# Kernel tuning notes

Measured on AMD Instinct MI355X. Metric: run time of the kernel, lower is better.

## Reference

```python
import jax, jax.numpy as jnp
import numpy as np

H = 16        # num_attention_heads
D = 1024      # hidden_size
HD = D // H   # attention_head_size = 64

def setup_inputs() -> dict:
    key = jax.random.key(0)
    ks = jax.random.split(key, 5)
    scale = 0.02
    return {
        "hidden_states": jax.random.normal(ks[0], (4, 2048, D), dtype=jnp.float32),
        "attention_mask": jnp.zeros((4, 2048), dtype=jnp.float32),
        "Wq": jax.random.normal(ks[1], (D, D), dtype=jnp.float32) * scale,
        "bq": jnp.zeros((D,), dtype=jnp.float32),
        "Wk": jax.random.normal(ks[2], (D, D), dtype=jnp.float32) * scale,
        "bk": jnp.zeros((D,), dtype=jnp.float32),
        "Wv": jax.random.normal(ks[3], (D, D), dtype=jnp.float32) * scale,
        "bv": jnp.zeros((D,), dtype=jnp.float32),
    }

def _heads(x, B, S):
    # [B,S,D] -> [B,H,S,HD]
    return x.reshape(B, S, H, HD).transpose(0, 2, 1, 3)

def reference(hidden_states, attention_mask, Wq, bq, Wk, bk, Wv, bv):
    B, S, _ = hidden_states.shape
    q = _heads(hidden_states @ Wq + bq, B, S)
    k = _heads(hidden_states @ Wk + bk, B, S)
    v = _heads(hidden_states @ Wv + bv, B, S)
    # scores: [B,H,S,S]
    scores = jnp.einsum('bhqd,bhkd->bhqk', q, k) / jnp.sqrt(jnp.float32(HD))
    scores = scores + attention_mask[:, None, None, :]  # additive mask
    probs = jax.nn.softmax(scores, axis=-1)
    # dropout is identity in eval mode
    ctx = jnp.einsum('bhqk,bhkd->bhqd', probs, v)
    return ctx.transpose(0, 2, 1, 3).reshape(B, S, H * HD)
```

## Files before the change

kernel.cpp:

```cpp
#include <hip/hip_runtime.h>


typedef __bf16 bf16_t;
typedef __bf16 bf16x2 __attribute__((ext_vector_type(2)));
typedef __bf16 bf16x4 __attribute__((ext_vector_type(4)));
typedef __bf16 bf16x8 __attribute__((ext_vector_type(8)));
typedef float floatx16 __attribute__((ext_vector_type(16)));
typedef float floatx4 __attribute__((ext_vector_type(4)));
typedef float floatx2 __attribute__((ext_vector_type(2)));

__device__ __forceinline__ void glds16(const void* g, void* l) {
  __builtin_amdgcn_global_load_lds(
      (const __attribute__((address_space(1))) void*)g,
      (__attribute__((address_space(3))) void*)l, 16, 0, 0);
}

__device__ __forceinline__ float exp2_fast(float x) {
  return __builtin_amdgcn_exp2f(x);
}

__device__ __forceinline__ unsigned pk2(float a, float b) {
  union { bf16x2 v; unsigned u; } cv;
  cv.v[0] = (bf16_t)a; cv.v[1] = (bf16_t)b;
  return cv.u;
}

__device__ __forceinline__ void plane32(unsigned& a, unsigned& b) {
  asm("v_permlane32_swap_b32 %0, %1" : "+v"(a), "+v"(b));
}

__global__ __launch_bounds__(256) void k_prep(const float* __restrict__ X,
                                              bf16_t* __restrict__ Xb,
                                              const float* __restrict__ Wq,
                                              const float* __restrict__ Wk,
                                              const float* __restrict__ Wv,
                                              bf16_t* __restrict__ Wt) {
  int bid = blockIdx.x;
  if (bid < 8192) {
    int i = (bid * 256 + threadIdx.x) * 4;
    float4 v = *(const float4*)(X + i);
    bf16x4 o;
    o[0] = (bf16_t)v.x; o[1] = (bf16_t)v.y; o[2] = (bf16_t)v.z; o[3] = (bf16_t)v.w;
    *(bf16x4*)(Xb + i) = o;
  } else {
    int t = bid - 8192;
    int z = t >> 10, r2 = t & 1023;
    int bx = r2 & 31, by = r2 >> 5;
    const float* W = (z == 0) ? Wq : ((z == 1) ? Wk : Wv);
    bf16_t* dst = Wt + (size_t)z * 1048576;
    __shared__ float tt[32][33];
    int tx = threadIdx.x & 31, ty = threadIdx.x >> 5;
#pragma unroll
    for (int r = 0; r < 4; r++) {
      int k = by * 32 + ty + r * 8;
      tt[ty + r * 8][tx] = W[k * 1024 + bx * 32 + tx];
    }
    __syncthreads();
#pragma unroll
    for (int r = 0; r < 4; r++) {
      int n = bx * 32 + ty + r * 8;
      dst[(size_t)n * 1024 + by * 32 + tx] = (bf16_t)tt[tx][ty + r * 8];
    }
  }
}

#define QKV_STAGE_A(kt, slot)                                 \
  do {                                                        \
    bf16_t* sA_ = lds + (slot) * 24576;                       \
    bf16_t* sB_ = sA_ + 8192;                                 \
    glds16(gA0 + (kt) * 64, sA_ + dA0);                       \
    glds16(gA1 + (kt) * 64, sA_ + dA1);                       \
    glds16(gB0 + (kt) * 64, sB_ + dB0);                       \
  } while (0)
#define QKV_STAGE_B(kt, slot)                                 \
  do {                                                        \
    bf16_t* sA_ = lds + (slot) * 24576;                       \
    bf16_t* sB_ = sA_ + 8192;                                 \
    glds16(gB1 + (kt) * 64, sB_ + dB1);                       \
    glds16(gB2 + (kt) * 64, sB_ + dB2);                       \
    glds16(gB3 + (kt) * 64, sB_ + dB3);                       \
  } while (0)

__global__ __launch_bounds__(512, 2) void k_qkv(
    const bf16_t* __restrict__ Xb, const bf16_t* __restrict__ Wt,
    const float* __restrict__ bq, const float* __restrict__ bk,
    const float* __restrict__ bv, bf16_t* __restrict__ Qb,
    bf16_t* __restrict__ Kb, bf16_t* __restrict__ Vt) {
  extern __shared__ bf16_t lds[];
  int tid = threadIdx.x, wv = tid >> 6, lane = tid & 63;
  int wvv = wv & 3, half = wv >> 2;
  int quad = lane >> 4, l16 = lane & 15;
  int wm = wvv >> 1, wn = wvv & 1;

  int id = blockIdx.x;
  int x = id & 7, w = id >> 3;
  int bn = w >> 3, pm = w & 7;
  int bm = x * 8 + pm;
  size_t m0 = (size_t)bm * 128, n0 = (size_t)bn * 256;
  int wsel = bn >> 2;

  const bf16_t* Ab = Xb + m0 * 1024;
  const bf16_t* Bb = Wt + n0 * 1024;

  const bf16_t *gA0, *gA1, *gB0, *gB1, *gB2, *gB3;
  int dA0, dA1, dB0, dB1, dB2, dB3;
  {
    int r8 = lane >> 3, l8 = lane & 7;
    int jA0 = wv * 2, jA1 = wv * 2 + 1;
    int rA0 = jA0 * 8 + r8, rA1 = jA1 * 8 + r8;
    gA0 = Ab + (size_t)rA0 * 1024 + ((l8 ^ (rA0 & 7)) * 8);
    gA1 = Ab + (size_t)rA1 * 1024 + ((l8 ^ (rA1 & 7)) * 8);
    dA0 = jA0 * 512; dA1 = jA1 * 512;
    int jB = wv * 4;
    int rB0 = (jB + 0) * 8 + r8, rB1 = (jB + 1) * 8 + r8;
    int rB2 = (jB + 2) * 8 + r8, rB3 = (jB + 3) * 8 + r8;
    gB0 = Bb + (size_t)rB0 * 1024 + ((l8 ^ (rB0 & 7)) * 8);
    gB1 = Bb + (size_t)rB1 * 1024 + ((l8 ^ (rB1 & 7)) * 8);
    gB2 = Bb + (size_t)rB2 * 1024 + ((l8 ^ (rB2 & 7)) * 8);
    gB3 = Bb + (size_t)rB3 * 1024 + ((l8 ^ (rB3 & 7)) * 8);
    dB0 = (jB + 0) * 512; dB1 = (jB + 1) * 512;
    dB2 = (jB + 2) * 512; dB3 = (jB + 3) * 512;
  }

  int ofsA[2][4], ofsB[2][4];
#pragma unroll
  for (int s = 0; s < 2; s++)
#pragma unroll
    for (int rt = 0; rt < 4; rt++) {
      int rowa = wm * 64 + rt * 16 + l16;
      ofsA[s][rt] = rowa * 64 + (((4 * s + quad) ^ (rowa & 7)) * 8);
      int rowb = wn * 64 + rt * 16 + l16;
      ofsB[s][rt] = rowb * 64 + (((4 * s + quad) ^ (rowb & 7)) * 8);
    }

  floatx4 acc[4][4];
#pragma unroll
  for (int a = 0; a < 4; a++)
#pragma unroll
    for (int b = 0; b < 4; b++)
#pragma unroll
      for (int r = 0; r < 4; r++) acc[a][b][r] = 0.f;

  QKV_STAGE_A(0, 0); QKV_STAGE_B(0, 0);
  QKV_STAGE_A(1, 1); QKV_STAGE_B(1, 1);

#pragma unroll
  for (int t = 0; t < 16; ++t) {
    asm volatile("" ::: "memory");
    __builtin_amdgcn_s_barrier();
    if (t < 15) asm volatile("s_waitcnt vmcnt(6)" ::: "memory");
    else        asm volatile("s_waitcnt vmcnt(0)" ::: "memory");
    __builtin_amdgcn_sched_barrier(0);
    __builtin_amdgcn_s_barrier();
    asm volatile("" ::: "memory");

    const bf16_t* sA = lds + (t % 3) * 24576;
    const bf16_t* sBh = sA + 8192 + half * 8192;
    const bf16_t* fA = (wsel == 2) ? sBh : sA;
    const bf16_t* fB = (wsel == 2) ? sA : sBh;

    if (t + 2 < 16) QKV_STAGE_A(t + 2, (t + 2) % 3);
    {
      bf16x8 av[4], bw[4];
#pragma unroll
      for (int rt = 0; rt < 4; rt++) {
        av[rt] = *(const bf16x8*)(fA + ofsA[0][rt]);
        bw[rt] = *(const bf16x8*)(fB + ofsB[0][rt]);
      }
      __builtin_amdgcn_s_setprio(1);
#pragma unroll
      for (int rt = 0; rt < 4; rt++)
#pragma unroll
        for (int ct = 0; ct < 4; ct++)
          acc[rt][ct] = __builtin_amdgcn_mfma_f32_16x16x32_bf16(av[rt], bw[ct],
                                                               acc[rt][ct], 0, 0, 0);
      __builtin_amdgcn_s_setprio(0);
    }
    asm volatile("" ::: "memory");
    __builtin_amdgcn_s_barrier();
    asm volatile("" ::: "memory");

    if (t + 2 < 16) QKV_STAGE_B(t + 2, (t + 2) % 3);
    {
      bf16x8 av[4], bw[4];
#pragma unroll
      for (int rt = 0; rt < 4; rt++) {
        av[rt] = *(const bf16x8*)(fA + ofsA[1][rt]);
        bw[rt] = *(const bf16x8*)(fB + ofsB[1][rt]);
      }
      __builtin_amdgcn_s_setprio(1);
#pragma unroll
      for (int rt = 0; rt < 4; rt++)
#pragma unroll
        for (int ct = 0; ct < 4; ct++)
          acc[rt][ct] = __builtin_amdgcn_mfma_f32_16x16x32_bf16(av[rt], bw[ct],
                                                               acc[rt][ct], 0, 0, 0);
      __builtin_amdgcn_s_setprio(0);
    }
  }

  __syncthreads();
  bf16_t* shC = lds + half * 16384;
  int s0 = (int)(m0 & 2047), bb = (int)(m0 >> 11);
  int n0h = (int)(n0 & 1023) + half * 128;
  int hbase = n0h >> 6;
  int th = tid & 255;

  if (wsel == 2) {
#pragma unroll
    for (int rt = 0; rt < 4; rt++) {
#pragma unroll
      for (int r = 0; r < 4; r++) {
        int nl = wm * 64 + rt * 16 + quad * 4 + r;
        float bi = bv[n0h + nl];
#pragma unroll
        for (int ct = 0; ct < 4; ct++) {
          int ml = wn * 64 + ct * 16 + l16;
          shC[nl * 128 + ml] = (bf16_t)(acc[rt][ct][r] + bi);
        }
      }
    }
    __syncthreads();
#pragma unroll
    for (int p = 0; p < 8; p++) {
      int c = p * 256 + th;
      int nl = c >> 4, mo = (c & 15) * 8;
      bf16x8 vv = *(const bf16x8*)(shC + nl * 128 + mo);
      int hh = hbase + (nl >> 6), dd = nl & 63;
      *(bf16x8*)(Vt + (size_t)(bb * 16 + hh) * 131072 + (size_t)dd * 2048 + s0 + mo) = vv;
    }
  } else {
    const float* bias = (wsel == 0) ? bq : bk;
#pragma unroll
    for (int ct = 0; ct < 4; ct++) {
      int nl = wn * 64 + ct * 16 + l16;
      float bi = bias[n0h + nl];
#pragma unroll
      for (int rt = 0; rt < 4; rt++) {
#pragma unroll
        for (int r = 0; r < 4; r++) {
          int ml = wm * 64 + rt * 16 + quad * 4 + r;
          float v = acc[rt][ct][r] + bi;
          shC[ml * 128 + nl] =
              (wsel == 0) ? (bf16_t)(v * 0.18033688011117f) : (bf16_t)v;
        }
      }
    }
    __syncthreads();
    bf16_t* outp = (wsel == 0) ? Qb : Kb;
#pragma unroll
    for (int p = 0; p < 8; p++) {
      int c = p * 256 + th;
      int h = c >> 10, c1 = c & 1023;
      int ml = c1 >> 3, ko = (c1 & 7) * 8;
      bf16x8 vv = *(const bf16x8*)(shC + ml * 128 + h * 64 + ko);
      *(bf16x8*)(outp + (size_t)(bb * 16 + hbase + h) * 131072 +
                 (size_t)(s0 + ml) * 64 + ko) = vv;
    }
  }
}

__global__ __launch_bounds__(256, 2) void k_attn(const bf16_t* __restrict__ Qb,
                                                 const bf16_t* __restrict__ Kb,
                                                 const bf16_t* __restrict__ VtG,
                                                 const float* __restrict__ mask,
                                                 float* __restrict__ out) {
  __shared__ float smem[10240];
  bf16_t* lds = (bf16_t*)smem;
  float* mlds = smem + 8192;

  int tid = threadIdx.x, wq = tid >> 6, lane = tid & 63;
  int q5 = lane & 31, h5 = lane >> 5;

  int id = blockIdx.x;
  int x = id & 7, w = id >> 3;
  int bh = x * 8 + (w >> 3), qt = w & 7;
  int b = bh >> 4, hh = bh & 15;

  const bf16_t* Qp = Qb + (size_t)bh * 131072;
  const bf16_t* Kp = Kb + (size_t)bh * 131072;
  const bf16_t* Vp = VtG + (size_t)bh * 131072;
  const float* mp = mask + b * 2048;

#pragma unroll
  for (int j = 0; j < 2; j++) {
    float4 mv = *(const float4*)(mp + tid * 8 + j * 4);
    float4 sv;
    sv.x = mv.x * 1.4426950408890f - 12.0f;
    sv.y = mv.y * 1.4426950408890f - 12.0f;
    sv.z = mv.z * 1.4426950408890f - 12.0f;
    sv.w = mv.w * 1.4426950408890f - 12.0f;
    *(float4*)(mlds + tid * 8 + j * 4) = sv;
  }

  int q0 = qt * 256 + wq * 64;
  bf16x8 qf0[4], qf1[4];
#pragma unroll
  for (int s = 0; s < 4; s++) {
    qf0[s] = *(const bf16x8*)(Qp + (size_t)(q0 + q5) * 64 + s * 16 + h5 * 8);
    qf1[s] = *(const bf16x8*)(Qp + (size_t)(q0 + 32 + q5) * 64 + s * 16 + h5 * 8);
  }

  union { uint4 u; bf16x8 v; } qfe;
  qfe.u.x = h5 ? 0u : 0x00003f80u;
  qfe.u.y = 0u; qfe.u.z = 0u; qfe.u.w = 0u;

  int off[2][4];
#pragma unroll
  for (int j = 0; j < 2; j++)
#pragma unroll
    for (int s = 0; s < 4; s++)
      off[j][s] = (j * 32 + q5) * 64 + (((2 * s + h5) ^ (q5 & 7)) * 8);

  int r0 = wq * 16 + (lane >> 3);
  int slot = (lane & 7) ^ ((lane >> 3) & 7);
  const bf16_t* kg0 = Kp + (size_t)r0 * 64 + slot * 8;
  const bf16_t* kg1 = kg0 + 512;
  const bf16_t* vg0 = Vp + (size_t)r0 * 2048 + slot * 8;
  const bf16_t* vg1 = vg0 + 16384;
  int c0 = wq * 2;

  floatx16 zed;
#pragma unroll
  for (int r = 0; r < 16; r++) zed[r] = 0.f;

  floatx16 ov[4];
#pragma unroll
  for (int t2 = 0; t2 < 4; t2++)
#pragma unroll
    for (int r = 0; r < 16; r++) ov[t2][r] = 0.f;
  floatx2 pA0, pA1, pB0, pB1;
  pA0[0] = pA0[1] = pA1[0] = pA1[1] = 0.f;
  pB0[0] = pB0[1] = pB1[0] = pB1[1] = 0.f;

  {
    bf16_t* bK = lds;
    bf16_t* bV = lds + 4096;
    glds16(kg0, bK + c0 * 512); glds16(kg1, bK + c0 * 512 + 512);
    glds16(vg0, bV + c0 * 512); glds16(vg1, bV + c0 * 512 + 512);
    kg0 += 4096; kg1 += 4096; vg0 += 64; vg1 += 64;
  }

  for (int it = 0; it < 32; ++it) {
    int kk0 = it * 64, cur = it & 1;
    __syncthreads();
    if (it + 1 < 32) {
      bf16_t* bK = lds + (cur ^ 1) * 8192;
      bf16_t* bV = bK + 4096;
      glds16(kg0, bK + c0 * 512); glds16(kg1, bK + c0 * 512 + 512);
      glds16(vg0, bV + c0 * 512); glds16(vg1, bV + c0 * 512 + 512);
      kg0 += 4096; kg1 += 4096; vg0 += 64; vg1 += 64;
    }
    const bf16_t* bK = lds + cur * 8192;
    const bf16_t* bV = bK + 4096;

    union { uint4 u; bf16x8 v; } kfe[2];
    kfe[0].u.x = h5 ? 0u : pk2(mlds[kk0 + q5], 0.f);
    kfe[1].u.x = h5 ? 0u : pk2(mlds[kk0 + 32 + q5], 0.f);
    kfe[0].u.y = 0u; kfe[0].u.z = 0u; kfe[0].u.w = 0u;
    kfe[1].u.y = 0u; kfe[1].u.z = 0u; kfe[1].u.w = 0u;

#pragma unroll
    for (int tt = 0; tt < 2; tt++) {
      bf16x8 kf[4], vfa[2], vfb[2];
#pragma unroll
      for (int s = 0; s < 4; s++) kf[s] = *(const bf16x8*)(bK + off[tt][s]);
#pragma unroll
      for (int t2 = 0; t2 < 2; t2++) {
        vfa[t2] = *(const bf16x8*)(bV + off[t2][tt * 2]);
        vfb[t2] = *(const bf16x8*)(bV + off[t2][tt * 2 + 1]);
      }

      floatx16 a0, a1;
      __builtin_amdgcn_s_setprio(1);
      floatx16 mt = __builtin_amdgcn_mfma_f32_32x32x16_bf16(kfe[tt].v, qfe.v, zed, 0, 0, 0);
      a0 = __builtin_amdgcn_mfma_f32_32x32x16_bf16(kf[0], qf0[0], mt, 0, 0, 0);
      a1 = __builtin_amdgcn_mfma_f32_32x32x16_bf16(kf[0], qf1[0], mt, 0, 0, 0);
#pragma unroll
      for (int s = 1; s < 4; s++) {
        a0 = __builtin_amdgcn_mfma_f32_32x32x16_bf16(kf[s], qf0[s], a0, 0, 0, 0);
        a1 = __builtin_amdgcn_mfma_f32_32x32x16_bf16(kf[s], qf1[s], a1, 0, 0, 0);
      }
      __builtin_amdgcn_s_setprio(0);

#pragma unroll
      for (int sl = 0; sl < 2; sl++) {
        int base = sl * 8;
        float e0 = exp2_fast(a0[base + 0]);
        float e1 = exp2_fast(a0[base + 1]);
        float e2 = exp2_fast(a0[base + 2]);
        float e3 = exp2_fast(a0[base + 3]);
        float e4 = exp2_fast(a0[base + 4]);
        float e5 = exp2_fast(a0[base + 5]);
        float e6 = exp2_fast(a0[base + 6]);
        float e7 = exp2_fast(a0[base + 7]);
        floatx2 u0, u1;
        u0[0] = e0 + e4; u0[1] = e1 + e5; pA0 += u0;
        u1[0] = e2 + e6; u1[1] = e3 + e7; pA1 += u1;
        unsigned A0 = pk2(e0, e1), B0 = pk2(e2, e3);
        unsigned C0 = pk2(e4, e5), D0 = pk2(e6, e7);
        float f0 = exp2_fast(a1[base + 0]);
        float f1 = exp2_fast(a1[base + 1]);
        float f2 = exp2_fast(a1[base + 2]);
        float f3 = exp2_fast(a1[base + 3]);
        float f4 = exp2_fast(a1[base + 4]);
        float f5 = exp2_fast(a1[base + 5]);
        float f6 = exp2_fast(a1[base + 6]);
        float f7 = exp2_fast(a1[base + 7]);
        floatx2 w0, w1;
        w0[0] = f0 + f4; w0[1] = f1 + f5; pB0 += w0;
        w1[0] = f2 + f6; w1[1] = f3 + f7; pB1 += w1;
        unsigned A1 = pk2(f0, f1), B1 = pk2(f2, f3);
        unsigned C1 = pk2(f4, f5), D1 = pk2(f6, f7);
        unsigned px0 = A0, pz0 = C0; plane32(px0, pz0);
        unsigned py0 = B0, pw0 = D0; plane32(py0, pw0);
        unsigned px1 = A1, pz1 = C1; plane32(px1, pz1);
        unsigned py1 = B1, pw1 = D1; plane32(py1, pw1);
        union { uint4 u; bf16x8 v; } pf0, pf1;
        pf0.u.x = px0; pf0.u.y = py0; pf0.u.z = pz0; pf0.u.w = pw0;
        pf1.u.x = px1; pf1.u.y = py1; pf1.u.z = pz1; pf1.u.w = pw1;
        __builtin_amdgcn_s_setprio(1);
#pragma unroll
        for (int t2 = 0; t2 < 2; t2++) {
          bf16x8 vf = sl ? vfb[t2] : vfa[t2];
          ov[t2]     = __builtin_amdgcn_mfma_f32_32x32x16_bf16(vf, pf0.v, ov[t2], 0, 0, 0);
          ov[2 + t2] = __builtin_amdgcn_mfma_f32_32x32x16_bf16(vf, pf1.v, ov[2 + t2], 0, 0, 0);
        }
        __builtin_amdgcn_s_setprio(0);
      }
    }
  }

  float ls0 = (pA0[0] + pA0[1]) + (pA1[0] + pA1[1]);
  float ls1 = (pB0[0] + pB0[1]) + (pB1[0] + pB1[1]);
  ls0 += __shfl_xor(ls0, 32);
  ls1 += __shfl_xor(ls1, 32);
  float rl0 = 1.f / ls0, rl1 = 1.f / ls1;

  int qbase0 = b * 2048 + qt * 256;
#pragma unroll
  for (int half = 0; half < 2; half++) {
    __syncthreads();
    if ((wq >> 1) == half) {
      int qw = (wq & 1) * 64;
#pragma unroll
      for (int u = 0; u < 2; u++) {
        float rl = u ? rl1 : rl0;
#pragma unroll
        for (int t2 = 0; t2 < 2; t2++)
#pragma unroll
          for (int r = 0; r < 16; r++) {
            int d = t2 * 32 + (r & 3) + 8 * (r >> 2) + 4 * h5;
            smem[(qw + u * 32 + q5) * 68 + d] = ov[u * 2 + t2][r] * rl;
          }
      }
    }
    __syncthreads();
    int qbase = qbase0 + half * 128;
#pragma unroll
    for (int i = 0; i < 8; i++) {
      int slot2 = i * 256 + tid;
      int q = slot2 >> 4, c = slot2 & 15;
      float4 v = *(const float4*)(smem + q * 68 + c * 4);
      *(float4*)(out + (size_t)(qbase + q) * 1024 + hh * 64 + c * 4) = v;
    }
  }
}

extern "C" void kernel_launch(void* const* d_in, const int* in_sizes, int n_in,
                              void* d_out, int out_size, void* d_ws, size_t ws_size,
                              hipStream_t stream) {
  const float* X    = (const float*)d_in[0];
  const float* mask = (const float*)d_in[1];
  const float* Wq   = (const float*)d_in[2];
  const float* bq   = (const float*)d_in[3];
  const float* Wk   = (const float*)d_in[4];
  const float* bk   = (const float*)d_in[5];
  const float* Wv   = (const float*)d_in[6];
  const float* bv   = (const float*)d_in[7];
  float* out = (float*)d_out;

  char* ws = (char*)d_ws;
  bf16_t* Xb = (bf16_t*)ws;
  bf16_t* Wt = (bf16_t*)(ws + 16777216);
  bf16_t* Qb = (bf16_t*)(ws + 23068672);
  bf16_t* Kb = (bf16_t*)(ws + 39845888);
  bf16_t* Vt = (bf16_t*)(ws + 56623104);

  k_prep<<<11264, 256, 0, stream>>>(X, Xb, Wq, Wk, Wv, Wt);
  k_qkv<<<768, 512, 147456, stream>>>(Xb, Wt, bq, bk, bv, Qb, Kb, Vt);
  k_attn<<<512, 256, 0, stream>>>(Qb, Kb, Vt, mask, out);
}
```

Baseline: 224.5 us.

## Software-pipeline QK^T and softmax-PV across half-tiles in attention loop

Restructures the attention main loop so the QK^T MFMAs for one 32-key half-tile are issued before the exp/pack/PV work of the previous half-tile. This uses a prologue, a steady state that alternates two score register sets, and an epilogue. The aim is to overlap the exp2 and bf16 packing VALU work with MFMA execution instead of serialising them. It keeps more live accumulator and V-fragment registers, which could raise register pressure or cause spills at the 2-blocks-per-CU launch bound.

```diff
diff --git a/kernel.cpp b/kernel.cpp
--- a/kernel.cpp
+++ b/kernel.cpp
@@ -260,6 +260,80 @@
   }
 }
 
+
+#define QKHALF(TT, A0R, A1R, VFA, VFB)                                        \
+  do {                                                                        \
+    bf16x8 kf_[4];                                                            \
+    _Pragma("unroll")                                                         \
+    for (int s_ = 0; s_ < 4; s_++)                                            \
+      kf_[s_] = *(const bf16x8*)(bK + off[TT][s_]);                           \
+    _Pragma("unroll")                                                         \
+    for (int t2_ = 0; t2_ < 2; t2_++) {                                       \
+      (VFA)[t2_] = *(const bf16x8*)(bV + off[t2_][(TT) * 2]);                 \
+      (VFB)[t2_] = *(const bf16x8*)(bV + off[t2_][(TT) * 2 + 1]);             \
+    }                                                                         \
+    __builtin_amdgcn_s_setprio(1);                                            \
+    floatx16 mt_ = __builtin_amdgcn_mfma_f32_32x32x16_bf16(kfe[TT].v, qfe.v,  \
+                                                           zed, 0, 0, 0);     \
+    (A0R) = __builtin_amdgcn_mfma_f32_32x32x16_bf16(kf_[0], qf0[0], mt_, 0, 0, 0); \
+    (A1R) = __builtin_amdgcn_mfma_f32_32x32x16_bf16(kf_[0], qf1[0], mt_, 0, 0, 0); \
+    _Pragma("unroll")                                                         \
+    for (int s_ = 1; s_ < 4; s_++) {                                          \
+      (A0R) = __builtin_amdgcn_mfma_f32_32x32x16_bf16(kf_[s_], qf0[s_], (A0R), 0, 0, 0); \
+      (A1R) = __builtin_amdgcn_mfma_f32_32x32x16_bf16(kf_[s_], qf1[s_], (A1R), 0, 0, 0); \
+    }                                                                         \
+    __builtin_amdgcn_s_setprio(0);                                            \
+  } while (0)
+
+#define SMPV(A0R, A1R, VFA, VFB)                                              \
+  do {                                                                        \
+    _Pragma("unroll")                                                         \
+    for (int sl_ = 0; sl_ < 2; sl_++) {                                       \
+      int base_ = sl_ * 8;                                                    \
+      float e0 = exp2_fast((A0R)[base_ + 0]);                                 \
+      float e1 = exp2_fast((A0R)[base_ + 1]);                                 \
+      float e2 = exp2_fast((A0R)[base_ + 2]);                                 \
+      float e3 = exp2_fast((A0R)[base_ + 3]);                                 \
+      float e4 = exp2_fast((A0R)[base_ + 4]);                                 \
+      float e5 = exp2_fast((A0R)[base_ + 5]);                                 \
+      float e6 = exp2_fast((A0R)[base_ + 6]);                                 \
+      float e7 = exp2_fast((A0R)[base_ + 7]);                                 \
+      floatx2 u0_, u1_;                                                       \
+      u0_[0] = e0 + e4; u0_[1] = e1 + e5; pA0 += u0_;                         \
+      u1_[0] = e2 + e6; u1_[1] = e3 + e7; pA1 += u1_;                         \
+      unsigned A0_ = pk2(e0, e1), B0_ = pk2(e2, e3);                          \
+      unsigned C0_ = pk2(e4, e5), D0_ = pk2(e6, e7);                          \
+      float f0 = exp2_fast((A1R)[base_ + 0]);                                 \
+      float f1 = exp2_fast((A1R)[base_ + 1]);                                 \
+      float f2 = exp2_fast((A1R)[base_ + 2]);                                 \
+      float f3 = exp2_fast((A1R)[base_ + 3]);                                 \
+      float f4 = exp2_fast((A1R)[base_ + 4]);                                 \
+      float f5 = exp2_fast((A1R)[base_ + 5]);                                 \
+      float f6 = exp2_fast((A1R)[base_ + 6]);                                 \
+      float f7 = exp2_fast((A1R)[base_ + 7]);                                 \
+      floatx2 w0_, w1_;                                                       \
+      w0_[0] = f0 + f4; w0_[1] = f1 + f5; pB0 += w0_;                         \
+      w1_[0] = f2 + f6; w1_[1] = f3 + f7; pB1 += w1_;                         \
+      unsigned A1_ = pk2(f0, f1), B1_ = pk2(f2, f3);                          \
+      unsigned C1_ = pk2(f4, f5), D1_ = pk2(f6, f7);                          \
+      unsigned px0 = A0_, pz0 = C0_; plane32(px0, pz0);                       \
+      unsigned py0 = B0_, pw0 = D0_; plane32(py0, pw0);                       \
+      unsigned px1 = A1_, pz1 = C1_; plane32(px1, pz1);                       \
+      unsigned py1 = B1_, pw1 = D1_; plane32(py1, pw1);                       \
+      union { uint4 u; bf16x8 v; } pf0_, pf1_;                                \
+      pf0_.u.x = px0; pf0_.u.y = py0; pf0_.u.z = pz0; pf0_.u.w = pw0;         \
+      pf1_.u.x = px1; pf1_.u.y = py1; pf1_.u.z = pz1; pf1_.u.w = pw1;         \
+      __builtin_amdgcn_s_setprio(1);                                          \
+      _Pragma("unroll")                                                       \
+      for (int t2_ = 0; t2_ < 2; t2_++) {                                     \
+        bf16x8 vf_ = sl_ ? (VFB)[t2_] : (VFA)[t2_];                           \
+        ov[t2_]     = __builtin_amdgcn_mfma_f32_32x32x16_bf16(vf_, pf0_.v, ov[t2_], 0, 0, 0); \
+        ov[2 + t2_] = __builtin_amdgcn_mfma_f32_32x32x16_bf16(vf_, pf1_.v, ov[2 + t2_], 0, 0, 0); \
+      }                                                                       \
+      __builtin_amdgcn_s_setprio(0);                                          \
+    }                                                                         \
+  } while (0)
+
 __global__ __launch_bounds__(256, 2) void k_attn(const bf16_t* __restrict__ Qb,
                                                  const bf16_t* __restrict__ Kb,
                                                  const bf16_t* __restrict__ VtG,
@@ -333,6 +407,9 @@
   pA0[0] = pA0[1] = pA1[0] = pA1[1] = 0.f;
   pB0[0] = pB0[1] = pB1[0] = pB1[1] = 0.f;
 
+  floatx16 aA0, aA1, aB0, aB1;
+  bf16x8 vfaA[2], vfbA[2], vfaB[2], vfbB[2];
+
   {
     bf16_t* bK = lds;
     bf16_t* bV = lds + 4096;
@@ -341,7 +418,30 @@
     kg0 += 4096; kg1 += 4096; vg0 += 64; vg1 += 64;
   }
 
-  for (int it = 0; it < 32; ++it) {
+  {
+    __syncthreads();
+    {
+      bf16_t* bK = lds + 8192;
+      bf16_t* bV = bK + 4096;
+      glds16(kg0, bK + c0 * 512); glds16(kg1, bK + c0 * 512 + 512);
+      glds16(vg0, bV + c0 * 512); glds16(vg1, bV + c0 * 512 + 512);
+      kg0 += 4096; kg1 += 4096; vg0 += 64; vg1 += 64;
+    }
+    const bf16_t* bK = lds;
+    const bf16_t* bV = bK + 4096;
+
+    union { uint4 u; bf16x8 v; } kfe[2];
+    kfe[0].u.x = h5 ? 0u : pk2(mlds[q5], 0.f);
+    kfe[1].u.x = h5 ? 0u : pk2(mlds[32 + q5], 0.f);
+    kfe[0].u.y = 0u; kfe[0].u.z = 0u; kfe[0].u.w = 0u;
+    kfe[1].u.y = 0u; kfe[1].u.z = 0u; kfe[1].u.w = 0u;
+
+    QKHALF(0, aA0, aA1, vfaA, vfbA);
+    QKHALF(1, aB0, aB1, vfaB, vfbB);
+    SMPV(aA0, aA1, vfaA, vfbA);
+  }
+
+  for (int it = 1; it < 32; ++it) {
     int kk0 = it * 64, cur = it & 1;
     __syncthreads();
     if (it + 1 < 32) {
@@ -360,76 +460,12 @@
     kfe[0].u.y = 0u; kfe[0].u.z = 0u; kfe[0].u.w = 0u;
     kfe[1].u.y = 0u; kfe[1].u.z = 0u; kfe[1].u.w = 0u;
 
-#pragma unroll
-    for (int tt = 0; tt < 2; tt++) {
-      bf16x8 kf[4], vfa[2], vfb[2];
-#pragma unroll
-      for (int s = 0; s < 4; s++) kf[s] = *(const bf16x8*)(bK + off[tt][s]);
-#pragma unroll
-      for (int t2 = 0; t2 < 2; t2++) {
-        vfa[t2] = *(const bf16x8*)(bV + off[t2][tt * 2]);
-        vfb[t2] = *(const bf16x8*)(bV + off[t2][tt * 2 + 1]);
-      }
-
-      floatx16 a0, a1;
-      __builtin_amdgcn_s_setprio(1);
-      floatx16 mt = __builtin_amdgcn_mfma_f32_32x32x16_bf16(kfe[tt].v, qfe.v, zed, 0, 0, 0);
-      a0 = __builtin_amdgcn_mfma_f32_32x32x16_bf16(kf[0], qf0[0], mt, 0, 0, 0);
-      a1 = __builtin_amdgcn_mfma_f32_32x32x16_bf16(kf[0], qf1[0], mt, 0, 0, 0);
-#pragma unroll
-      for (int s = 1; s < 4; s++) {
-        a0 = __builtin_amdgcn_mfma_f32_32x32x16_bf16(kf[s], qf0[s], a0, 0, 0, 0);
-        a1 = __builtin_amdgcn_mfma_f32_32x32x16_bf16(kf[s], qf1[s], a1, 0, 0, 0);
-      }
-      __builtin_amdgcn_s_setprio(0);
-
-#pragma unroll
-      for (int sl = 0; sl < 2; sl++) {
-        int base = sl * 8;
-        float e0 = exp2_fast(a0[base + 0]);
-        float e1 = exp2_fast(a0[base + 1]);
-        float e2 = exp2_fast(a0[base + 2]);
-        float e3 = exp2_fast(a0[base + 3]);
-        float e4 = exp2_fast(a0[base + 4]);
-        float e5 = exp2_fast(a0[base + 5]);
-        float e6 = exp2_fast(a0[base + 6]);
-        float e7 = exp2_fast(a0[base + 7]);
-        floatx2 u0, u1;
-        u0[0] = e0 + e4; u0[1] = e1 + e5; pA0 += u0;
-        u1[0] = e2 + e6; u1[1] = e3 + e7; pA1 += u1;
-        unsigned A0 = pk2(e0, e1), B0 = pk2(e2, e3);
-        unsigned C0 = pk2(e4, e5), D0 = pk2(e6, e7);
-        float f0 = exp2_fast(a1[base + 0]);
-        float f1 = exp2_fast(a1[base + 1]);
-        float f2 = exp2_fast(a1[base + 2]);
-        float f3 = exp2_fast(a1[base + 3]);
-        float f4 = exp2_fast(a1[base + 4]);
-        float f5 = exp2_fast(a1[base + 5]);
-        float f6 = exp2_fast(a1[base + 6]);
-        float f7 = exp2_fast(a1[base + 7]);
-        floatx2 w0, w1;
-        w0[0] = f0 + f4; w0[1] = f1 + f5; pB0 += w0;
-        w1[0] = f2 + f6; w1[1] = f3 + f7; pB1 += w1;
-        unsigned A1 = pk2(f0, f1), B1 = pk2(f2, f3);
-        unsigned C1 = pk2(f4, f5), D1 = pk2(f6, f7);
-        unsigned px0 = A0, pz0 = C0; plane32(px0, pz0);
-        unsigned py0 = B0, pw0 = D0; plane32(py0, pw0);
-        unsigned px1 = A1, pz1 = C1; plane32(px1, pz1);
-        unsigned py1 = B1, pw1 = D1; plane32(py1, pw1);
-        union { uint4 u; bf16x8 v; } pf0, pf1;
-        pf0.u.x = px0; pf0.u.y = py0; pf0.u.z = pz0; pf0.u.w = pw0;
-        pf1.u.x = px1; pf1.u.y = py1; pf1.u.z = pz1; pf1.u.w = pw1;
-        __builtin_amdgcn_s_setprio(1);
-#pragma unroll
-        for (int t2 = 0; t2 < 2; t2++) {
-          bf16x8 vf = sl ? vfb[t2] : vfa[t2];
-          ov[t2]     = __builtin_amdgcn_mfma_f32_32x32x16_bf16(vf, pf0.v, ov[t2], 0, 0, 0);
-          ov[2 + t2] = __builtin_amdgcn_mfma_f32_32x32x16_bf16(vf, pf1.v, ov[2 + t2], 0, 0, 0);
-        }
-        __builtin_amdgcn_s_setprio(0);
-      }
-    }
-  }
+    QKHALF(0, aA0, aA1, vfaA, vfbA);
+    SMPV(aB0, aB1, vfaB, vfbB);
+    QKHALF(1, aB0, aB1, vfaB, vfbB);
+    SMPV(aA0, aA1, vfaA, vfbA);
+  }
+  SMPV(aB0, aB1, vfaB, vfbB);
 
   float ls0 = (pA0[0] + pA0[1]) + (pA1[0] + pA1[1]);
   float ls1 = (pB0[0] + pB0[1]) + (pB1[0] + pB1[1]);
```

Result: slower. 231.8 us (+3.2%).

## Split attention key range across two wave groups per block and merge partial outputs

Applied to the files above, without the earlier changes.

The attention kernel now launches 512 threads per block. Two groups of four waves each handle half of the 2048 keys for the same query tile, with separate double-buffered K/V LDS regions. The row sums are exchanged through LDS, and the two partial outputs are added in shared memory before writeback. The goal is more waves in flight per CU and shorter serial key loops. The cost is extra LDS, extra syncs and a serial merge step. The fixed softmax offset with no running max makes the merge a simple sum.

```diff
diff --git a/kernel.cpp b/kernel.cpp
--- a/kernel.cpp
+++ b/kernel.cpp
@@ -260,16 +260,18 @@
   }
 }
 
-__global__ __launch_bounds__(256, 2) void k_attn(const bf16_t* __restrict__ Qb,
+__global__ __launch_bounds__(512, 4) void k_attn(const bf16_t* __restrict__ Qb,
                                                  const bf16_t* __restrict__ Kb,
                                                  const bf16_t* __restrict__ VtG,
                                                  const float* __restrict__ mask,
                                                  float* __restrict__ out) {
-  __shared__ float smem[10240];
+  __shared__ float smem[18944];
   bf16_t* lds = (bf16_t*)smem;
-  float* mlds = smem + 8192;
+  float* mlds = smem + 16384;
+  float* lsbuf = smem + 18432;
 
   int tid = threadIdx.x, wq = tid >> 6, lane = tid & 63;
+  int wsub = wq & 3, kv = wq >> 2;
   int q5 = lane & 31, h5 = lane >> 5;
 
   int id = blockIdx.x;
@@ -282,18 +284,17 @@
   const bf16_t* Vp = VtG + (size_t)bh * 131072;
   const float* mp = mask + b * 2048;
 
-#pragma unroll
-  for (int j = 0; j < 2; j++) {
-    float4 mv = *(const float4*)(mp + tid * 8 + j * 4);
+  {
+    float4 mv = *(const float4*)(mp + tid * 4);
     float4 sv;
     sv.x = mv.x * 1.4426950408890f - 12.0f;
     sv.y = mv.y * 1.4426950408890f - 12.0f;
     sv.z = mv.z * 1.4426950408890f - 12.0f;
     sv.w = mv.w * 1.4426950408890f - 12.0f;
-    *(float4*)(mlds + tid * 8 + j * 4) = sv;
-  }
-
-  int q0 = qt * 256 + wq * 64;
+    *(float4*)(mlds + tid * 4) = sv;
+  }
+
+  int q0 = qt * 256 + wsub * 64;
   bf16x8 qf0[4], qf1[4];
 #pragma unroll
   for (int s = 0; s < 4; s++) {
@@ -312,13 +313,14 @@
     for (int s = 0; s < 4; s++)
       off[j][s] = (j * 32 + q5) * 64 + (((2 * s + h5) ^ (q5 & 7)) * 8);
 
-  int r0 = wq * 16 + (lane >> 3);
+  int kb = kv << 10;
+  int r0 = wsub * 16 + (lane >> 3);
   int slot = (lane & 7) ^ ((lane >> 3) & 7);
-  const bf16_t* kg0 = Kp + (size_t)r0 * 64 + slot * 8;
+  const bf16_t* kg0 = Kp + (size_t)(kb + r0) * 64 + slot * 8;
   const bf16_t* kg1 = kg0 + 512;
-  const bf16_t* vg0 = Vp + (size_t)r0 * 2048 + slot * 8;
+  const bf16_t* vg0 = Vp + (size_t)r0 * 2048 + kb + slot * 8;
   const bf16_t* vg1 = vg0 + 16384;
-  int c0 = wq * 2;
+  int c0 = wsub * 2;
 
   floatx16 zed;
 #pragma unroll
@@ -334,24 +336,24 @@
   pB0[0] = pB0[1] = pB1[0] = pB1[1] = 0.f;
 
   {
-    bf16_t* bK = lds;
-    bf16_t* bV = lds + 4096;
+    bf16_t* bK = lds + kv * 8192;
+    bf16_t* bV = bK + 4096;
     glds16(kg0, bK + c0 * 512); glds16(kg1, bK + c0 * 512 + 512);
     glds16(vg0, bV + c0 * 512); glds16(vg1, bV + c0 * 512 + 512);
     kg0 += 4096; kg1 += 4096; vg0 += 64; vg1 += 64;
   }
 
-  for (int it = 0; it < 32; ++it) {
-    int kk0 = it * 64, cur = it & 1;
-    __syncthreads();
-    if (it + 1 < 32) {
-      bf16_t* bK = lds + (cur ^ 1) * 8192;
+  for (int it = 0; it < 16; ++it) {
+    int kk0 = kb + it * 64, cur = it & 1;
+    __syncthreads();
+    if (it + 1 < 16) {
+      bf16_t* bK = lds + (cur ^ 1) * 16384 + kv * 8192;
       bf16_t* bV = bK + 4096;
       glds16(kg0, bK + c0 * 512); glds16(kg1, bK + c0 * 512 + 512);
       glds16(vg0, bV + c0 * 512); glds16(vg1, bV + c0 * 512 + 512);
       kg0 += 4096; kg1 += 4096; vg0 += 64; vg1 += 64;
     }
-    const bf16_t* bK = lds + cur * 8192;
+    const bf16_t* bK = lds + cur * 16384 + kv * 8192;
     const bf16_t* bV = bK + 4096;
 
     union { uint4 u; bf16x8 v; } kfe[2];
@@ -435,14 +437,20 @@
   float ls1 = (pB0[0] + pB0[1]) + (pB1[0] + pB1[1]);
   ls0 += __shfl_xor(ls0, 32);
   ls1 += __shfl_xor(ls1, 32);
-  float rl0 = 1.f / ls0, rl1 = 1.f / ls1;
+  if (lane < 32) {
+    lsbuf[kv * 256 + wsub * 64 + q5] = ls0;
+    lsbuf[kv * 256 + wsub * 64 + 32 + q5] = ls1;
+  }
+  __syncthreads();
+  float rl0 = 1.f / (lsbuf[wsub * 64 + q5] + lsbuf[256 + wsub * 64 + q5]);
+  float rl1 = 1.f / (lsbuf[wsub * 64 + 32 + q5] + lsbuf[256 + wsub * 64 + 32 + q5]);
 
   int qbase0 = b * 2048 + qt * 256;
 #pragma unroll
   for (int half = 0; half < 2; half++) {
     __syncthreads();
-    if ((wq >> 1) == half) {
-      int qw = (wq & 1) * 64;
+    if ((wsub >> 1) == half && kv == 0) {
+      int qw = (wsub & 1) * 64;
 #pragma unroll
       for (int u = 0; u < 2; u++) {
         float rl = u ? rl1 : rl0;
@@ -456,10 +464,25 @@
       }
     }
     __syncthreads();
+    if ((wsub >> 1) == half && kv == 1) {
+      int qw = (wsub & 1) * 64;
+#pragma unroll
+      for (int u = 0; u < 2; u++) {
+        float rl = u ? rl1 : rl0;
+#pragma unroll
+        for (int t2 = 0; t2 < 2; t2++)
+#pragma unroll
+          for (int r = 0; r < 16; r++) {
+            int d = t2 * 32 + (r & 3) + 8 * (r >> 2) + 4 * h5;
+            smem[(qw + u * 32 + q5) * 68 + d] += ov[u * 2 + t2][r] * rl;
+          }
+      }
+    }
+    __syncthreads();
     int qbase = qbase0 + half * 128;
 #pragma unroll
-    for (int i = 0; i < 8; i++) {
-      int slot2 = i * 256 + tid;
+    for (int i = 0; i < 4; i++) {
+      int slot2 = i * 512 + tid;
       int q = slot2 >> 4, c = slot2 & 15;
       float4 v = *(const float4*)(smem + q * 68 + c * 4);
       *(float4*)(out + (size_t)(qbase + q) * 1024 + hh * 64 + c * 4) = v;
@@ -489,5 +512,5 @@
 
   k_prep<<<11264, 256, 0, stream>>>(X, Xb, Wq, Wk, Wv, Wt);
   k_qkv<<<768, 512, 147456, stream>>>(Xb, Wt, bq, bk, bv, Qb, Kb, Vt);
-  k_attn<<<512, 256, 0, stream>>>(Qb, Kb, Vt, mask, out);
-}
+  k_attn<<<512, 512, 0, stream>>>(Qb, Kb, Vt, mask, out);
+}
```

After: 673.0 us. +199.8%, slower.
